# Kernel optimization log

Measured on AMD Instinct MI355X. Metric: run time of the kernel, lower is better.

The kernel has to match this reference:

```python
import jax, jax.numpy as jnp
import numpy as np

K = 3  # conv1d kernel size
PAD = (K - 1) // 2


def _conv1d_1ch(x, w, b):
    # x: (B, 1, C), w: (1, 1, K), b: (1,)  -- torch Conv1d cross-correlation
    c = x.shape[-1]
    xp = jnp.pad(x, ((0, 0), (0, 0), (PAD, PAD)))
    y = sum(w[0, 0, k] * xp[:, :, k:k + c] for k in range(K))
    return y + b[0]


def setup_inputs() -> dict:
    key = jax.random.key(0)
    ks = jax.random.split(key, 13)
    B, C, H, W, E = 8, 256, 48, 48, 64
    s = lambda fan: 1.0 / np.sqrt(fan)
    return {
        "feature": jax.random.normal(ks[0], (B, C, H, W), jnp.float32),
        "wq1": jax.random.normal(ks[1], (1, 1, K), jnp.float32) * s(K),
        "bq1": jax.random.normal(ks[2], (1,), jnp.float32) * s(K),
        "wk1": jax.random.normal(ks[3], (1, 1, K), jnp.float32) * s(K),
        "bk1": jax.random.normal(ks[4], (1,), jnp.float32) * s(K),
        "wq2": jax.random.normal(ks[5], (E, C), jnp.float32) * s(C),
        "bq2": jax.random.normal(ks[6], (E,), jnp.float32) * s(C),
        "wk2": jax.random.normal(ks[7], (E, C), jnp.float32) * s(C),
        "bk2": jax.random.normal(ks[8], (E,), jnp.float32) * s(C),
        "wv2": jax.random.normal(ks[9], (E, C), jnp.float32) * s(C),
        "bv2": jax.random.normal(ks[10], (E,), jnp.float32) * s(C),
        "watt": jax.random.normal(ks[11], (C, E), jnp.float32) * s(E),
        "batt": jax.random.normal(ks[12], (C,), jnp.float32) * s(E),
    }


def reference(feature, wq1, bq1, wk1, bk1, wq2, bq2, wk2, bk2, wv2, bv2, watt, batt):
    b, c, h, w = feature.shape
    hw = h * w

    # ---- Global Channel Attention ----
    gap = jnp.mean(feature, axis=(2, 3)).reshape(b, 1, c)
    query = jax.nn.sigmoid(_conv1d_1ch(gap, wq1, bq1))  # (b,1,c)
    key_ = jax.nn.sigmoid(_conv1d_1ch(gap, wk1, bk1))   # (b,1,c)
    att_c = key_[:, 0, :, None] * query[:, 0, None, :]  # (b,c,c) = K^T Q
    att_c = jax.nn.softmax(att_c, axis=1)               # softmax over dim=1
    value = feature.reshape(b, hw, c)                   # raw reshape, as in torch
    gc = jnp.matmul(value, att_c).reshape(b, c, h, w)   # raw reshape back

    # ---- Global Spatial Attention ----
    q = (jnp.einsum('bchw,ec->behw', feature, wq2) + bq2[None, :, None, None]).reshape(b, -1, hw)
    k = (jnp.einsum('bchw,ec->behw', feature, wk2) + bk2[None, :, None, None]).reshape(b, -1, hw)
    v = (jnp.einsum('bchw,ec->behw', feature, wv2) + bv2[None, :, None, None]).reshape(b, -1, hw)
    att_s = jnp.einsum('bei,bej->bij', k, q)            # (b,hw,hw)
    att_s = jax.nn.softmax(att_s, axis=2)
    gs = jnp.einsum('bei,bij->bej', v, att_s).reshape(b, -1, h, w)  # (b,e,h,w)
    gs = jnp.einsum('behw,ce->bchw', gs, watt) + batt[None, :, None, None]

    # ---- Gated combination ----
    feature_gc = feature * gc
    return feature_gc * gs + feature_gc
```

## Files before the change

### kernel.cpp

```cpp
#include <hip/hip_runtime.h>

#define B_ 8
#define C_ 256
#define HW_ 2304
#define E_ 64
#define SB_ (C_*HW_)
#define LOG2E_ 1.44269504088896340736f

typedef unsigned short u16;
typedef __attribute__((ext_vector_type(8))) __bf16 bf16x8;
typedef __attribute__((ext_vector_type(4))) float f32x4;
typedef __attribute__((ext_vector_type(16))) float f32x16;
#define MFMA16(a,b,c) __builtin_amdgcn_mfma_f32_16x16x32_bf16(a,b,c,0,0,0)
#define MFMA32(a,b,c) __builtin_amdgcn_mfma_f32_32x32x16_bf16(a,b,c,0,0,0)

#define LDS_FENCE() do { asm volatile("s_waitcnt lgkmcnt(0)" ::: "memory"); \
                         __builtin_amdgcn_sched_barrier(0); } while(0)

#define PSWAP(a,b) asm("v_permlane32_swap_b32 %0, %1" : "+v"(a), "+v"(b))

static __device__ inline u16 f2bf(float x){
  unsigned u = __builtin_bit_cast(unsigned, x);
  u += 0x7FFFu + ((u >> 16) & 1u);
  return (u16)(u >> 16);
}
static __device__ inline float bf2f(u16 h){
  unsigned u = ((unsigned)h) << 16;
  return __builtin_bit_cast(float, u);
}
static __device__ __forceinline__ unsigned cvtpk_bf16(float a, float b){
  unsigned r;
  asm("v_cvt_pk_bf16_f32 %0, %1, %2" : "=v"(r) : "v"(a), "v"(b));
  return r;
}
static __device__ __forceinline__ void split2(float x0, float x1, unsigned &H, unsigned &L){
  H = cvtpk_bf16(x0, x1);
  float h0 = __builtin_bit_cast(float, H << 16);
  float h1 = __builtin_bit_cast(float, H & 0xFFFF0000u);
  L = cvtpk_bf16(x0 - h0, x1 - h1);
}


struct KFrag { bf16x8 h0, h1, l0, l1; };
static __device__ __forceinline__ KFrag ldfrag(const u16* __restrict__ ph,
                                               const u16* __restrict__ pl,
                                               size_t tile, int lane){
  KFrag q;
  q.h0 = *(const bf16x8*)(ph + (tile*2+0)*512 + (size_t)lane*8);
  q.h1 = *(const bf16x8*)(ph + (tile*2+1)*512 + (size_t)lane*8);
  q.l0 = *(const bf16x8*)(pl + (tile*2+0)*512 + (size_t)lane*8);
  q.l1 = *(const bf16x8*)(pl + (tile*2+1)*512 + (size_t)lane*8);
  return q;
}

__global__ __launch_bounds__(256) void k_gap(const float* __restrict__ f, float* __restrict__ gap){
  int bc = blockIdx.x;
  const float* row = f + (size_t)bc * HW_;
  float s = 0.f;
  for (int i = threadIdx.x; i < HW_; i += 256) s += row[i];
  #pragma unroll
  for (int off = 32; off; off >>= 1) s += __shfl_down(s, off);
  __shared__ float red[4];
  int lane = threadIdx.x & 63, wv = threadIdx.x >> 6;
  if (lane == 0) red[wv] = s;
  __syncthreads();
  if (threadIdx.x == 0) gap[bc] = (red[0]+red[1]+red[2]+red[3]) * (1.0f/HW_);
}

__global__ __launch_bounds__(256) void k_attc2(const float* __restrict__ gap,
    const float* __restrict__ wq1, const float* __restrict__ bq1,
    const float* __restrict__ wk1, const float* __restrict__ bk1,
    u16* __restrict__ ath, u16* __restrict__ atl){
  int b = blockIdx.x >> 8;
  int j = blockIdx.x & 255;
  int i = threadIdx.x;
  const float* g = gap + b*C_;
  float gm1 = (i > 0)      ? g[i-1] : 0.f;
  float g0  = g[i];
  float gp1 = (i < C_-1)   ? g[i+1] : 0.f;
  float keyv = wk1[0]*gm1 + wk1[1]*g0 + wk1[2]*gp1 + bk1[0];
  keyv = 1.f/(1.f+__expf(-keyv));
  float qm1 = (j > 0)      ? g[j-1] : 0.f;
  float q0  = g[j];
  float qp1 = (j < C_-1)   ? g[j+1] : 0.f;
  float qv = wq1[0]*qm1 + wq1[1]*q0 + wq1[2]*qp1 + bq1[0];
  qv = 1.f/(1.f+__expf(-qv));
  float s = keyv * qv;
  __shared__ float red[256];
  red[i] = s; __syncthreads();
  for (int st = 128; st > 0; st >>= 1){ if (i < st) red[i] = fmaxf(red[i], red[i+st]); __syncthreads(); }
  float mx = red[0]; __syncthreads();
  float e = __expf(s - mx);
  red[i] = e; __syncthreads();
  for (int st = 128; st > 0; st >>= 1){ if (i < st) red[i] += red[i+st]; __syncthreads(); }
  float sum = red[0];
  float x = e / sum;
  u16 hb = f2bf(x);
  size_t o = (((size_t)b*16 + (j>>4))*8 + (i>>5))*512 + (((i&31)>>3)*16 + (j&15))*8 + (i&7);
  ath[o] = hb;
  atl[o] = f2bf(x - bf2f(hb));
}

__global__ __launch_bounds__(256) void k_wcvt(const float* __restrict__ wq,
    const float* __restrict__ wk, const float* __restrict__ wv,
    u16* __restrict__ wbh, u16* __restrict__ wbl){
  int n = blockIdx.x*256 + threadIdx.x;
  int mz = n >> 14; int idx = n & 16383;
  int e = idx >> 8, c = idx & 255;
  const float* w = (mz==0) ? wq : ((mz==1) ? wk : wv);
  float x = w[idx] * ((mz==1) ? LOG2E_ : 1.0f);
  u16 hb = f2bf(x);
  size_t widx = (((size_t)mz*4 + (e>>4))*8 + (c>>5))*512 + (((c&31)>>3)*16 + (e&15))*8 + (c&7);
  wbh[widx] = hb;
  wbl[widx] = f2bf(x - bf2f(hb));
}

__global__ __launch_bounds__(256) void k_proj7(const float* __restrict__ f,
    const u16* __restrict__ wbh, const u16* __restrict__ wbl,
    const float* __restrict__ bq, const float* __restrict__ bk, const float* __restrict__ bv,
    u16* __restrict__ qh, u16* __restrict__ qlo,
    u16* __restrict__ kh, u16* __restrict__ klo,
    u16* __restrict__ vh, u16* __restrict__ vlo){
  int b = blockIdx.x;
  int wv = threadIdx.x >> 6;
  int py = blockIdx.y*4 + wv;
  int p0 = py*16;
  int mz = blockIdx.z >> 1, mh = blockIdx.z & 1;
  int lane = threadIdx.x & 63; int l15 = lane & 15, g = lane >> 4;
  const float* fb = f + (size_t)b*SB_ + p0 + l15;
  const u16* wh = wbh + (size_t)mz*16384;
  const u16* wl = wbl + (size_t)mz*16384;
  const float* bi = (mz==0) ? bq : ((mz==1) ? bk : bv);
  const float bsc = (mz==1) ? LOG2E_ : 1.0f;
  f32x4 c1[2], c2[2], c3[2];
  #pragma unroll
  for (int m = 0; m < 2; m++){
    c1[m] = (f32x4){0.f,0.f,0.f,0.f};
    c2[m] = (f32x4){0.f,0.f,0.f,0.f};
    c3[m] = (f32x4){0.f,0.f,0.f,0.f};
  }
  #pragma unroll
  for (int ks = 0; ks < 8; ks++){
    int cb = ks*32 + g*8;
    float fe[8];
    #pragma unroll
    for (int u = 0; u < 8; u++) fe[u] = fb[(size_t)(cb + u)*HW_];
    union { unsigned w[4]; bf16x8 v; } FH, FL;
    #pragma unroll
    for (int u = 0; u < 4; u++) split2(fe[2*u], fe[2*u+1], FH.w[u], FL.w[u]);
    #pragma unroll
    for (int ml = 0; ml < 2; ml++){
      int m = mh*2 + ml;
      bf16x8 awh = *(const bf16x8*)(wh + ((size_t)m*8 + ks)*512 + (size_t)lane*8);
      bf16x8 awl = *(const bf16x8*)(wl + ((size_t)m*8 + ks)*512 + (size_t)lane*8);
      c1[ml] = MFMA16(awh, FH.v, c1[ml]);
      c2[ml] = MFMA16(awh, FL.v, c2[ml]);
      c3[ml] = MFMA16(awl, FH.v, c3[ml]);
    }
  }
  if (mz < 2){
    u16* ohb = (mz==0 ? qh : kh);
    u16* olb = (mz==0 ? qlo: klo);
    size_t tb = ((size_t)b*144 + py)*2;
    #pragma unroll
    for (int ml = 0; ml < 2; ml++){
      int m = mh*2 + ml;
      float x0 = c1[ml][0]+c2[ml][0]+c3[ml][0] + bi[m*16+g*4+0]*bsc;
      float x1 = c1[ml][1]+c2[ml][1]+c3[ml][1] + bi[m*16+g*4+1]*bsc;
      float x2 = c1[ml][2]+c2[ml][2]+c3[ml][2] + bi[m*16+g*4+2]*bsc;
      float x3 = c1[ml][3]+c2[ml][3]+c3[ml][3] + bi[m*16+g*4+3]*bsc;
      union { unsigned w[2]; uint2 v2; } H, L;
      split2(x0, x1, H.w[0], L.w[0]);
      split2(x2, x3, H.w[1], L.w[1]);
      int kc = mh;
      int gc = ml*2 + (g >> 1);
      int ub = (g & 1)*4;
      size_t idx = (tb + kc)*512 + (gc*16 + l15)*8 + ub;
      *(uint2*)(ohb + idx) = H.v2;
      *(uint2*)(olb + idx) = L.v2;
    }
  } else {
    int ic = py >> 1;
    int half = py & 1;
    int gg = half*2 + (l15 >> 3);
    int uu = l15 & 7;
    size_t vb0 = ((size_t)b*72 + ic)*4;
    #pragma unroll
    for (int ml = 0; ml < 2; ml++){
      int m = mh*2 + ml;
      #pragma unroll
      for (int r = 0; r < 4; r++){
        int e = m*16 + g*4 + r;
        float x = c1[ml][r] + c2[ml][r] + c3[ml][r] + bi[e];
        u16 hb = f2bf(x);
        size_t idx = (vb0 + m)*512 + (gg*16 + (g*4 + r))*8 + uu;
        vh[idx] = hb;
        vlo[idx] = f2bf(x - bf2f(hb));
      }
    }
  }
}

__global__ __launch_bounds__(256) void k_stats7(
    const u16* __restrict__ qh, const u16* __restrict__ qlo,
    const u16* __restrict__ kh, const u16* __restrict__ klo,
    float* __restrict__ lpart){
  int b = blockIdx.x;
  int wv = threadIdx.x >> 6;
  int it0 = blockIdx.y*4 + wv;
  int jz = blockIdx.z;
  int lane = threadIdx.x & 63; int l15 = lane & 15, g = lane >> 4;
  const size_t b144 = (size_t)b*144;
  KFrag kf0 = ldfrag(kh, klo, b144 + it0*2,     lane);
  KFrag kf1 = ldfrag(kh, klo, b144 + it0*2 + 1, lane);
  float lsum[8];
  #pragma unroll
  for (int x = 0; x < 8; x++) lsum[x] = 0.f;
  size_t qb0 = b144 + jz*16;
  #pragma unroll
  for (int t = 0; t < 16; t++){
    KFrag q = ldfrag(qh, qlo, qb0 + t, lane);
    #pragma unroll
    for (int isub = 0; isub < 2; isub++){
      const KFrag& kf = isub ? kf1 : kf0;
      f32x4 c1 = {0.f,0.f,0.f,0.f}, c2 = {0.f,0.f,0.f,0.f}, c3 = {0.f,0.f,0.f,0.f};
      c1 = MFMA16(kf.h0, q.h0, c1);
      c2 = MFMA16(kf.h0, q.l0, c2);
      c3 = MFMA16(kf.l0, q.h0, c3);
      c1 = MFMA16(kf.h1, q.h1, c1);
      c2 = MFMA16(kf.h1, q.l1, c2);
      c3 = MFMA16(kf.l1, q.h1, c3);
      #pragma unroll
      for (int r = 0; r < 4; r++) lsum[isub*4+r] += __builtin_exp2f(c1[r] + c2[r] + c3[r]);
    }
  }
  #pragma unroll
  for (int mk = 1; mk < 16; mk <<= 1){
    #pragma unroll
    for (int x = 0; x < 8; x++) lsum[x] += __shfl_xor(lsum[x], mk);
  }
  if (l15 == 0){
    float* lp = lpart + ((size_t)jz*B_ + b)*HW_ + it0*32;
    #pragma unroll
    for (int isub = 0; isub < 2; isub++)
      #pragma unroll
      for (int r = 0; r < 4; r++) lp[isub*16 + g*4 + r] = lsum[isub*4+r];
  }
}

__global__ __launch_bounds__(256) void k_lrl9(const float* __restrict__ lpart, float* __restrict__ lrl){
  int i = blockIdx.x*256 + threadIdx.x;
  const int BH = B_*HW_;
  float s = 0.f;
  #pragma unroll
  for (int p = 0; p < 9; p++) s += lpart[(size_t)p*BH + i];
  lrl[i] = -__builtin_log2f(s);
}

__global__ __launch_bounds__(256) void k_gs9(
    const u16* __restrict__ qh, const u16* __restrict__ qlo,
    const u16* __restrict__ kh, const u16* __restrict__ klo,
    const u16* __restrict__ vh, const u16* __restrict__ vlo,
    const float* __restrict__ lrl, float* __restrict__ gsp){
  int b = blockIdx.x;
  int wv = threadIdx.x >> 6;
  int jt32 = blockIdx.y*4 + wv;
  int iz = blockIdx.z;
  int j0 = jt32*32;
  int lane = threadIdx.x & 63;
  int l31 = lane & 31, h = lane >> 5, l15q = lane & 15, lh = l31 >> 4;
  __shared__ __align__(16) float GT[4][2048];
  const size_t b144 = (size_t)b*144;
  bf16x8 qfh[4], qfl[4];
  size_t qtile = (b144 + jt32*2 + lh)*2;
  #pragma unroll
  for (int m = 0; m < 4; m++){
    size_t qa = (qtile + (m>>1))*512 + (size_t)((((m&1)*2 + h)*16 + l15q)*8);
    qfh[m] = *(const bf16x8*)(qh + qa);
    qfl[m] = *(const bf16x8*)(qlo + qa);
  }
  f32x16 acc0 = {}, acc1 = {};
  const float* lrlb = lrl + b*HW_;
  #pragma unroll 2
  for (int ic = 0; ic < 8; ic++){
    int i0c = iz*256 + ic*32;
    bf16x8 kfh[4], kfl[4];
    size_t ktile = (b144 + iz*16 + ic*2 + lh)*2;
    #pragma unroll
    for (int m = 0; m < 4; m++){
      size_t ka = (ktile + (m>>1))*512 + (size_t)((((m&1)*2 + h)*16 + l15q)*8);
      kfh[m] = *(const bf16x8*)(kh + ka);
      kfl[m] = *(const bf16x8*)(klo + ka);
    }
    bf16x8 vfh[2][2], vfl[2][2];
    size_t vslot = ((size_t)b*72 + iz*8 + ic)*4;
    #pragma unroll
    for (int eh = 0; eh < 2; eh++)
      #pragma unroll
      for (int n = 0; n < 2; n++){
        size_t va = (vslot + eh*2 + lh)*512 + (size_t)(((2*n + h)*16 + l15q)*8);
        vfh[eh][n] = *(const bf16x8*)(vh + va);
        vfl[eh][n] = *(const bf16x8*)(vlo + va);
      }
    f32x4 lr[4];
    #pragma unroll
    for (int rr = 0; rr < 4; rr++) lr[rr] = *(const f32x4*)&lrlb[i0c + rr*8 + 4*h];
    f32x16 c1 = {}, c23 = {};
    #pragma unroll
    for (int m = 0; m < 4; m++){
      c1  = MFMA32(kfh[m], qfh[m], c1);
      c23 = MFMA32(kfh[m], qfl[m], c23);
      c23 = MFMA32(kfl[m], qfh[m], c23);
    }
    unsigned Wh[8], Wl[8];
    #pragma unroll
    for (int w = 0; w < 8; w++){
      float p0 = __builtin_exp2f(c1[2*w]   + c23[2*w]   + lr[(2*w)>>2][(2*w)&3]);
      float p1 = __builtin_exp2f(c1[2*w+1] + c23[2*w+1] + lr[(2*w+1)>>2][(2*w+1)&3]);
      split2(p0, p1, Wh[w], Wl[w]);
    }
    PSWAP(Wh[0], Wh[2]); PSWAP(Wh[1], Wh[3]);
    PSWAP(Wh[4], Wh[6]); PSWAP(Wh[5], Wh[7]);
    PSWAP(Wl[0], Wl[2]); PSWAP(Wl[1], Wl[3]);
    PSWAP(Wl[4], Wl[6]); PSWAP(Wl[5], Wl[7]);
    union { unsigned w[4]; bf16x8 v; } ph0, ph1, pl0, pl1;
    ph0.w[0]=Wh[0]; ph0.w[1]=Wh[1]; ph0.w[2]=Wh[2]; ph0.w[3]=Wh[3];
    ph1.w[0]=Wh[4]; ph1.w[1]=Wh[5]; ph1.w[2]=Wh[6]; ph1.w[3]=Wh[7];
    pl0.w[0]=Wl[0]; pl0.w[1]=Wl[1]; pl0.w[2]=Wl[2]; pl0.w[3]=Wl[3];
    pl1.w[0]=Wl[4]; pl1.w[1]=Wl[5]; pl1.w[2]=Wl[6]; pl1.w[3]=Wl[7];
    acc0 = MFMA32(vfh[0][0], ph0.v, acc0);
    acc0 = MFMA32(vfh[0][0], pl0.v, acc0);
    acc0 = MFMA32(vfl[0][0], ph0.v, acc0);
    acc0 = MFMA32(vfh[0][1], ph1.v, acc0);
    acc0 = MFMA32(vfh[0][1], pl1.v, acc0);
    acc0 = MFMA32(vfl[0][1], ph1.v, acc0);
    acc1 = MFMA32(vfh[1][0], ph0.v, acc1);
    acc1 = MFMA32(vfh[1][0], pl0.v, acc1);
    acc1 = MFMA32(vfl[1][0], ph0.v, acc1);
    acc1 = MFMA32(vfh[1][1], ph1.v, acc1);
    acc1 = MFMA32(vfh[1][1], pl1.v, acc1);
    acc1 = MFMA32(vfl[1][1], ph1.v, acc1);
  }
  float* gt = &GT[wv][0];
  #pragma unroll
  for (int r = 0; r < 16; r++){
    int erow = (r&3) + 8*(r>>2) + 4*h;
    gt[erow*32 + l31]        = acc0[r];
    gt[(32 + erow)*32 + l31] = acc1[r];
  }
  LDS_FENCE();
  float* gb = gsp + ((size_t)iz*B_ + b)*E_*HW_;
  #pragma unroll
  for (int itx = 0; itx < 8; itx++){
    int n = (itx*64 + lane)*4;
    f32x4 vvv = *(const f32x4*)&gt[n];
    int e = n >> 5, jj = n & 31;
    *(f32x4*)&gb[(size_t)e*HW_ + j0 + jj] = vvv;
  }
}

__global__ __launch_bounds__(256) void k_gsum9(const float* __restrict__ gsp, float* __restrict__ gs){
  const size_t N = (size_t)B_*E_*HW_;
  size_t n = ((size_t)blockIdx.x*256 + threadIdx.x)*4;
  f32x4 s = *(const f32x4*)(gsp + n);
  #pragma unroll
  for (int p = 1; p < 9; p++) s += *(const f32x4*)(gsp + (size_t)p*N + n);
  *(f32x4*)(gs + n) = s;
}

__global__ __launch_bounds__(256) void k_gsout2(const float* __restrict__ gs,
    const float* __restrict__ watt, const float* __restrict__ batt,
    float* __restrict__ gsout){
  int b = blockIdx.x; int sc = blockIdx.y; int cc0 = blockIdx.z * 16;
  int s = sc*256 + threadIdx.x;
  const float* gb = gs + (size_t)b*E_*HW_ + s;
  float acc[16];
  #pragma unroll
  for (int x = 0; x < 16; x++) acc[x] = 0.f;
  for (int e = 0; e < E_; e++){
    float gv = gb[(size_t)e*HW_];
    #pragma unroll
    for (int x = 0; x < 16; x++) acc[x] += watt[(cc0+x)*E_ + e] * gv;
  }
  float* ob = gsout + (size_t)b*SB_ + (size_t)cc0*HW_ + s;
  #pragma unroll
  for (int x = 0; x < 16; x++) ob[(size_t)x*HW_] = acc[x] + batt[cc0 + x];
}

__global__ __launch_bounds__(256) void k_final6(const float* __restrict__ f,
    const u16* __restrict__ ath, const u16* __restrict__ atl,
    float* __restrict__ inout){
  int b = blockIdx.x;
  int wv = threadIdx.x >> 6;
  int sy = blockIdx.y*4 + wv;
  int s0 = sy*16;
  int z = blockIdx.z;
  int lane = threadIdx.x & 63; int l15 = lane & 15, g = lane >> 4;
  const float* fb = f + (size_t)b*SB_;
  bf16x8 Ah[8], Al[8];
  const float* arow = fb + (size_t)(s0 + l15)*C_;
  #pragma unroll
  for (int ks = 0; ks < 8; ks++){
    int cbase = ks*32 + g*8;
    float4 f4a = *(const float4*)&arow[cbase];
    float4 f4b = *(const float4*)&arow[cbase + 4];
    union { unsigned w[4]; bf16x8 v; } H, L;
    split2(f4a.x, f4a.y, H.w[0], L.w[0]);
    split2(f4a.z, f4a.w, H.w[1], L.w[1]);
    split2(f4b.x, f4b.y, H.w[2], L.w[2]);
    split2(f4b.z, f4b.w, H.w[3], L.w[3]);
    Ah[ks] = H.v; Al[ks] = L.v;
  }
  const u16* abz_h = ath + (size_t)b*65536;
  const u16* abz_l = atl + (size_t)b*65536;
  f32x4 acc[4];
  #pragma unroll
  for (int q = 0; q < 4; q++) acc[q] = (f32x4){0.f,0.f,0.f,0.f};
  #pragma unroll
  for (int q = 0; q < 4; q++){
    int jt = z*4 + q;
    #pragma unroll
    for (int ks = 0; ks < 8; ks++){
      bf16x8 Bh = *(const bf16x8*)(abz_h + ((size_t)jt*8 + ks)*512 + (size_t)lane*8);
      bf16x8 Bl = *(const bf16x8*)(abz_l + ((size_t)jt*8 + ks)*512 + (size_t)lane*8);
      acc[q] = MFMA16(Ah[ks], Bh, acc[q]);
      acc[q] = MFMA16(Ah[ks], Bl, acc[q]);
      acc[q] = MFMA16(Al[ks], Bh, acc[q]);
    }
  }
  float* ob = inout + (size_t)b*SB_;
  #pragma unroll
  for (int q = 0; q < 4; q++){
    #pragma unroll
    for (int r = 0; r < 4; r++){
      int p = s0 + g*4 + r;
      int j = (z*4+q)*16 + l15;
      size_t n = (size_t)p*C_ + j;
      float fx = fb[n];
      float gso = ob[n];
      ob[n] = acc[q][r] * fx * (gso + 1.f);
    }
  }
}

extern "C" void kernel_launch(void* const* d_in, const int* in_sizes, int n_in,
                              void* d_out, int out_size, void* d_ws, size_t ws_size,
                              hipStream_t stream){
  const float* f    = (const float*)d_in[0];
  const float* wq1  = (const float*)d_in[1];
  const float* bq1  = (const float*)d_in[2];
  const float* wk1  = (const float*)d_in[3];
  const float* bk1  = (const float*)d_in[4];
  const float* wq2  = (const float*)d_in[5];
  const float* bq2  = (const float*)d_in[6];
  const float* wk2  = (const float*)d_in[7];
  const float* bk2  = (const float*)d_in[8];
  const float* wv2  = (const float*)d_in[9];
  const float* bv2  = (const float*)d_in[10];
  const float* watt = (const float*)d_in[11];
  const float* batt = (const float*)d_in[12];
  float* out = (float*)d_out;
  char* W = (char*)d_ws;

  float* gap   = (float*)(W + 0);
  u16*   ath   = (u16*)  (W + 8192);
  u16*   atl   = (u16*)  (W + 1056768);
  float* lpart = (float*)(W + 2105344);
  float* lrl   = (float*)(W + 2768896);
  float* gsp   = (float*)(W + 2842624);
  float* gs    = (float*)(W + 45309952);
  u16* qh  = (u16*)(W + 50028544);
  u16* qlo = (u16*)(W + 52387840);
  u16* kh  = (u16*)(W + 54747136);
  u16* klo = (u16*)(W + 57106432);
  u16* vh  = (u16*)(W + 59465728);
  u16* vlo = (u16*)(W + 61825024);
  u16* wbh = (u16*)(W + 64184320);
  u16* wbl = (u16*)(W + 64282624);

  k_gap   <<<B_*C_,             256, 0, stream>>>(f, gap);
  k_attc2 <<<B_*C_,             256, 0, stream>>>(gap, wq1, bq1, wk1, bk1, ath, atl);
  k_wcvt  <<<192,               256, 0, stream>>>(wq2, wk2, wv2, wbh, wbl);
  k_proj7 <<<dim3(B_, 36, 6),   256, 0, stream>>>(f, wbh, wbl, bq2, bk2, bv2,
                                                  qh, qlo, kh, klo, vh, vlo);
  k_stats7<<<dim3(B_, 18, 9),   256, 0, stream>>>(qh, qlo, kh, klo, lpart);
  k_lrl9  <<<B_*HW_/256,        256, 0, stream>>>(lpart, lrl);
  k_gs9   <<<dim3(B_, 18, 9),   256, 0, stream>>>(qh, qlo, kh, klo, vh, vlo, lrl, gsp);
  k_gsum9 <<<B_*E_*HW_/1024,    256, 0, stream>>>(gsp, gs);
  k_gsout2<<<dim3(B_, 9, 16),   256, 0, stream>>>(gs, watt, batt, out);
  k_final6<<<dim3(B_, 36, 4),   256, 0, stream>>>(f, ath, atl, out);
}
```

Baseline: 173.0 us.

## Retile spatial attention kernels: 64-wide tiles, 16x16 MFMA, LDS-staged P

The stats kernel now has each wave cover 64 rows of K instead of 32, so every loaded Q fragment is reused across four K tiles and the grid shrinks. The gs kernel is rewritten to use single-wave blocks over 64 query columns with 16x16x32 MFMAs. The softmax probabilities are staged through double-buffered LDS in place of the permlane32 swaps, and each K/V fragment is reused across four Q tiles. This aims to cut redundant global fragment loads. In exchange it adds LDS traffic, more registers per wave and a different occupancy profile.

Measured after the change: 181.3 us. +4.8%, slower.

```diff
diff --git a/kernel.cpp b/kernel.cpp
--- a/kernel.cpp
+++ b/kernel.cpp
@@ -16,8 +16,6 @@
 
 #define LDS_FENCE() do { asm volatile("s_waitcnt lgkmcnt(0)" ::: "memory"); \
                          __builtin_amdgcn_sched_barrier(0); } while(0)
-
-#define PSWAP(a,b) asm("v_permlane32_swap_b32 %0, %1" : "+v"(a), "+v"(b))
 
 static __device__ inline u16 f2bf(float x){
   unsigned u = __builtin_bit_cast(unsigned, x);
@@ -201,35 +199,36 @@
   }
 }
 
-__global__ __launch_bounds__(256) void k_stats7(
+__global__ __launch_bounds__(256) void k_stats8(
     const u16* __restrict__ qh, const u16* __restrict__ qlo,
     const u16* __restrict__ kh, const u16* __restrict__ klo,
     float* __restrict__ lpart){
   int b = blockIdx.x;
   int wv = threadIdx.x >> 6;
-  int it0 = blockIdx.y*4 + wv;
+  int it64 = blockIdx.y*4 + wv;
   int jz = blockIdx.z;
   int lane = threadIdx.x & 63; int l15 = lane & 15, g = lane >> 4;
   const size_t b144 = (size_t)b*144;
-  KFrag kf0 = ldfrag(kh, klo, b144 + it0*2,     lane);
-  KFrag kf1 = ldfrag(kh, klo, b144 + it0*2 + 1, lane);
-  float lsum[8];
-  #pragma unroll
-  for (int x = 0; x < 8; x++) lsum[x] = 0.f;
+  KFrag kf[4];
+  #pragma unroll
+  for (int isub = 0; isub < 4; isub++)
+    kf[isub] = ldfrag(kh, klo, b144 + it64*4 + isub, lane);
+  float lsum[16];
+  #pragma unroll
+  for (int x = 0; x < 16; x++) lsum[x] = 0.f;
   size_t qb0 = b144 + jz*16;
   #pragma unroll
   for (int t = 0; t < 16; t++){
     KFrag q = ldfrag(qh, qlo, qb0 + t, lane);
     #pragma unroll
-    for (int isub = 0; isub < 2; isub++){
-      const KFrag& kf = isub ? kf1 : kf0;
+    for (int isub = 0; isub < 4; isub++){
       f32x4 c1 = {0.f,0.f,0.f,0.f}, c2 = {0.f,0.f,0.f,0.f}, c3 = {0.f,0.f,0.f,0.f};
-      c1 = MFMA16(kf.h0, q.h0, c1);
-      c2 = MFMA16(kf.h0, q.l0, c2);
-      c3 = MFMA16(kf.l0, q.h0, c3);
-      c1 = MFMA16(kf.h1, q.h1, c1);
-      c2 = MFMA16(kf.h1, q.l1, c2);
-      c3 = MFMA16(kf.l1, q.h1, c3);
+      c1 = MFMA16(kf[isub].h0, q.h0, c1);
+      c2 = MFMA16(kf[isub].h0, q.l0, c2);
+      c3 = MFMA16(kf[isub].l0, q.h0, c3);
+      c1 = MFMA16(kf[isub].h1, q.h1, c1);
+      c2 = MFMA16(kf[isub].h1, q.l1, c2);
+      c3 = MFMA16(kf[isub].l1, q.h1, c3);
       #pragma unroll
       for (int r = 0; r < 4; r++) lsum[isub*4+r] += __builtin_exp2f(c1[r] + c2[r] + c3[r]);
     }
@@ -237,12 +236,12 @@
   #pragma unroll
   for (int mk = 1; mk < 16; mk <<= 1){
     #pragma unroll
-    for (int x = 0; x < 8; x++) lsum[x] += __shfl_xor(lsum[x], mk);
+    for (int x = 0; x < 16; x++) lsum[x] += __shfl_xor(lsum[x], mk);
   }
   if (l15 == 0){
-    float* lp = lpart + ((size_t)jz*B_ + b)*HW_ + it0*32;
-    #pragma unroll
-    for (int isub = 0; isub < 2; isub++)
+    float* lp = lpart + ((size_t)jz*B_ + b)*HW_ + it64*64;
+    #pragma unroll
+    for (int isub = 0; isub < 4; isub++)
       #pragma unroll
       for (int r = 0; r < 4; r++) lp[isub*16 + g*4 + r] = lsum[isub*4+r];
   }
@@ -257,105 +256,93 @@
   lrl[i] = -__builtin_log2f(s);
 }
 
-__global__ __launch_bounds__(256) void k_gs9(
+__global__ __launch_bounds__(64) void k_gs10(
     const u16* __restrict__ qh, const u16* __restrict__ qlo,
     const u16* __restrict__ kh, const u16* __restrict__ klo,
     const u16* __restrict__ vh, const u16* __restrict__ vlo,
     const float* __restrict__ lrl, float* __restrict__ gsp){
-  int b = blockIdx.x;
-  int wv = threadIdx.x >> 6;
-  int jt32 = blockIdx.y*4 + wv;
-  int iz = blockIdx.z;
-  int j0 = jt32*32;
-  int lane = threadIdx.x & 63;
-  int l31 = lane & 31, h = lane >> 5, l15q = lane & 15, lh = l31 >> 4;
-  __shared__ __align__(16) float GT[4][2048];
+  int b = blockIdx.x; int y = blockIdx.y; int iz = blockIdx.z;
+  int j0 = y*64;
+  int lane = threadIdx.x; int l15 = lane & 15, g = lane >> 4;
+  __shared__ __align__(16) char smem[20480];
   const size_t b144 = (size_t)b*144;
-  bf16x8 qfh[4], qfl[4];
-  size_t qtile = (b144 + jt32*2 + lh)*2;
-  #pragma unroll
-  for (int m = 0; m < 4; m++){
-    size_t qa = (qtile + (m>>1))*512 + (size_t)((((m&1)*2 + h)*16 + l15q)*8);
-    qfh[m] = *(const bf16x8*)(qh + qa);
-    qfl[m] = *(const bf16x8*)(qlo + qa);
-  }
-  f32x16 acc0 = {}, acc1 = {};
+  KFrag qf[4];
+  #pragma unroll
+  for (int jt = 0; jt < 4; jt++) qf[jt] = ldfrag(qh, qlo, b144 + y*4 + jt, lane);
+  f32x4 gacc[4][4];
+  #pragma unroll
+  for (int jt = 0; jt < 4; jt++)
+    #pragma unroll
+    for (int es = 0; es < 4; es++) gacc[jt][es] = (f32x4){0.f,0.f,0.f,0.f};
   const float* lrlb = lrl + b*HW_;
   #pragma unroll 2
   for (int ic = 0; ic < 8; ic++){
     int i0c = iz*256 + ic*32;
-    bf16x8 kfh[4], kfl[4];
-    size_t ktile = (b144 + iz*16 + ic*2 + lh)*2;
-    #pragma unroll
-    for (int m = 0; m < 4; m++){
-      size_t ka = (ktile + (m>>1))*512 + (size_t)((((m&1)*2 + h)*16 + l15q)*8);
-      kfh[m] = *(const bf16x8*)(kh + ka);
-      kfl[m] = *(const bf16x8*)(klo + ka);
-    }
-    bf16x8 vfh[2][2], vfl[2][2];
-    size_t vslot = ((size_t)b*72 + iz*8 + ic)*4;
-    #pragma unroll
-    for (int eh = 0; eh < 2; eh++)
-      #pragma unroll
-      for (int n = 0; n < 2; n++){
-        size_t va = (vslot + eh*2 + lh)*512 + (size_t)(((2*n + h)*16 + l15q)*8);
-        vfh[eh][n] = *(const bf16x8*)(vh + va);
-        vfl[eh][n] = *(const bf16x8*)(vlo + va);
+    char* PhB = smem + (ic & 1)*5120;
+    char* PlB = smem + 10240 + (ic & 1)*5120;
+    bf16x8 vfh[4], vfl[4];
+    #pragma unroll
+    for (int msub = 0; msub < 2; msub++){
+      KFrag kf = ldfrag(kh, klo, b144 + iz*16 + ic*2 + msub, lane);
+      f32x4 rlv = *(const f32x4*)&lrlb[i0c + msub*16 + g*4];
+      #pragma unroll
+      for (int jt = 0; jt < 4; jt++){
+        f32x4 c1 = {0.f,0.f,0.f,0.f}, c2 = {0.f,0.f,0.f,0.f}, c3 = {0.f,0.f,0.f,0.f};
+        c1 = MFMA16(kf.h0, qf[jt].h0, c1);
+        c2 = MFMA16(kf.h0, qf[jt].l0, c2);
+        c3 = MFMA16(kf.l0, qf[jt].h0, c3);
+        c1 = MFMA16(kf.h1, qf[jt].h1, c1);
+        c2 = MFMA16(kf.h1, qf[jt].l1, c2);
+        c3 = MFMA16(kf.l1, qf[jt].h1, c3);
+        float p0 = __builtin_exp2f(c1[0] + c2[0] + c3[0] + rlv[0]);
+        float p1 = __builtin_exp2f(c1[1] + c2[1] + c3[1] + rlv[1]);
+        float p2 = __builtin_exp2f(c1[2] + c2[2] + c3[2] + rlv[2]);
+        float p3 = __builtin_exp2f(c1[3] + c2[3] + c3[3] + rlv[3]);
+        union { unsigned w[2]; uint2 v2; } PH, PL;
+        split2(p0, p1, PH.w[0], PL.w[0]);
+        split2(p2, p3, PH.w[1], PL.w[1]);
+        *(uint2*)(PhB + (jt*16 + l15)*80 + msub*32 + g*8) = PH.v2;
+        *(uint2*)(PlB + (jt*16 + l15)*80 + msub*32 + g*8) = PL.v2;
       }
-    f32x4 lr[4];
-    #pragma unroll
-    for (int rr = 0; rr < 4; rr++) lr[rr] = *(const f32x4*)&lrlb[i0c + rr*8 + 4*h];
-    f32x16 c1 = {}, c23 = {};
-    #pragma unroll
-    for (int m = 0; m < 4; m++){
-      c1  = MFMA32(kfh[m], qfh[m], c1);
-      c23 = MFMA32(kfh[m], qfl[m], c23);
-      c23 = MFMA32(kfl[m], qfh[m], c23);
-    }
-    unsigned Wh[8], Wl[8];
-    #pragma unroll
-    for (int w = 0; w < 8; w++){
-      float p0 = __builtin_exp2f(c1[2*w]   + c23[2*w]   + lr[(2*w)>>2][(2*w)&3]);
-      float p1 = __builtin_exp2f(c1[2*w+1] + c23[2*w+1] + lr[(2*w+1)>>2][(2*w+1)&3]);
-      split2(p0, p1, Wh[w], Wl[w]);
-    }
-    PSWAP(Wh[0], Wh[2]); PSWAP(Wh[1], Wh[3]);
-    PSWAP(Wh[4], Wh[6]); PSWAP(Wh[5], Wh[7]);
-    PSWAP(Wl[0], Wl[2]); PSWAP(Wl[1], Wl[3]);
-    PSWAP(Wl[4], Wl[6]); PSWAP(Wl[5], Wl[7]);
-    union { unsigned w[4]; bf16x8 v; } ph0, ph1, pl0, pl1;
-    ph0.w[0]=Wh[0]; ph0.w[1]=Wh[1]; ph0.w[2]=Wh[2]; ph0.w[3]=Wh[3];
-    ph1.w[0]=Wh[4]; ph1.w[1]=Wh[5]; ph1.w[2]=Wh[6]; ph1.w[3]=Wh[7];
-    pl0.w[0]=Wl[0]; pl0.w[1]=Wl[1]; pl0.w[2]=Wl[2]; pl0.w[3]=Wl[3];
-    pl1.w[0]=Wl[4]; pl1.w[1]=Wl[5]; pl1.w[2]=Wl[6]; pl1.w[3]=Wl[7];
-    acc0 = MFMA32(vfh[0][0], ph0.v, acc0);
-    acc0 = MFMA32(vfh[0][0], pl0.v, acc0);
-    acc0 = MFMA32(vfl[0][0], ph0.v, acc0);
-    acc0 = MFMA32(vfh[0][1], ph1.v, acc0);
-    acc0 = MFMA32(vfh[0][1], pl1.v, acc0);
-    acc0 = MFMA32(vfl[0][1], ph1.v, acc0);
-    acc1 = MFMA32(vfh[1][0], ph0.v, acc1);
-    acc1 = MFMA32(vfh[1][0], pl0.v, acc1);
-    acc1 = MFMA32(vfl[1][0], ph0.v, acc1);
-    acc1 = MFMA32(vfh[1][1], ph1.v, acc1);
-    acc1 = MFMA32(vfh[1][1], pl1.v, acc1);
-    acc1 = MFMA32(vfl[1][1], ph1.v, acc1);
-  }
-  float* gt = &GT[wv][0];
-  #pragma unroll
-  for (int r = 0; r < 16; r++){
-    int erow = (r&3) + 8*(r>>2) + 4*h;
-    gt[erow*32 + l31]        = acc0[r];
-    gt[(32 + erow)*32 + l31] = acc1[r];
-  }
+      if (msub == 0){
+        size_t vc = ((size_t)b*72 + iz*8 + ic)*4;
+        #pragma unroll
+        for (int es = 0; es < 4; es++){
+          vfh[es] = *(const bf16x8*)(vh  + (vc+es)*512 + (size_t)lane*8);
+          vfl[es] = *(const bf16x8*)(vlo + (vc+es)*512 + (size_t)lane*8);
+        }
+      }
+    }
+    LDS_FENCE();
+    #pragma unroll
+    for (int jt = 0; jt < 4; jt++){
+      bf16x8 pf_h = *(const bf16x8*)(PhB + (jt*16 + l15)*80 + g*16);
+      bf16x8 pf_l = *(const bf16x8*)(PlB + (jt*16 + l15)*80 + g*16);
+      #pragma unroll
+      for (int es = 0; es < 4; es++){
+        gacc[jt][es] = MFMA16(vfh[es], pf_h, gacc[jt][es]);
+        gacc[jt][es] = MFMA16(vfh[es], pf_l, gacc[jt][es]);
+        gacc[jt][es] = MFMA16(vfl[es], pf_h, gacc[jt][es]);
+      }
+    }
+  }
+  LDS_FENCE();
+  float* GT = (float*)smem;
+  #pragma unroll
+  for (int jt = 0; jt < 4; jt++)
+    #pragma unroll
+    for (int es = 0; es < 4; es++)
+      #pragma unroll
+      for (int r = 0; r < 4; r++)
+        GT[(es*16 + g*4 + r)*64 + jt*16 + l15] = gacc[jt][es][r];
   LDS_FENCE();
   float* gb = gsp + ((size_t)iz*B_ + b)*E_*HW_;
   #pragma unroll
-  for (int itx = 0; itx < 8; itx++){
+  for (int itx = 0; itx < 16; itx++){
     int n = (itx*64 + lane)*4;
-    f32x4 vvv = *(const f32x4*)&gt[n];
-    int e = n >> 5, jj = n & 31;
-    *(f32x4*)&gb[(size_t)e*HW_ + j0 + jj] = vvv;
+    f32x4 vv = *(const f32x4*)&GT[n];
+    int e = n >> 6, jj = n & 63;
+    *(f32x4*)&gb[(size_t)e*HW_ + j0 + jj] = vv;
   }
 }
 
@@ -483,9 +470,9 @@
   k_wcvt  <<<192,               256, 0, stream>>>(wq2, wk2, wv2, wbh, wbl);
   k_proj7 <<<dim3(B_, 36, 6),   256, 0, stream>>>(f, wbh, wbl, bq2, bk2, bv2,
                                                   qh, qlo, kh, klo, vh, vlo);
-  k_stats7<<<dim3(B_, 18, 9),   256, 0, stream>>>(qh, qlo, kh, klo, lpart);
+  k_stats8<<<dim3(B_, 9, 9),    256, 0, stream>>>(qh, qlo, kh, klo, lpart);
   k_lrl9  <<<B_*HW_/256,        256, 0, stream>>>(lpart, lrl);
-  k_gs9   <<<dim3(B_, 18, 9),   256, 0, stream>>>(qh, qlo, kh, klo, vh, vlo, lrl, gsp);
+  k_gs10  <<<dim3(B_, 36, 9),    64, 0, stream>>>(qh, qlo, kh, klo, vh, vlo, lrl, gsp);
   k_gsum9 <<<B_*E_*HW_/1024,    256, 0, stream>>>(gsp, gs);
   k_gsout2<<<dim3(B_, 9, 16),   256, 0, stream>>>(gs, watt, batt, out);
   k_final6<<<dim3(B_, 36, 4),   256, 0, stream>>>(f, ath, atl, out);
```
